# Kernel tuning notes

Hardware: AMD Instinct MI355X
Metric: run time of the kernel (lower is better)

The kernel has to match this reference:

```python
import jax, jax.numpy as jnp
import numpy as np

B, TX, TZ, DX, DZ, DATT, DMID, H, DOUT = 8, 1024, 1024, 1024, 1024, 64, 64, 16, 1024


def setup_inputs() -> dict:
    key = jax.random.key(0)
    ks = jax.random.split(key, 10)
    s = 0.02
    return {
        "x": jax.random.normal(ks[0], (B, TX, DX), jnp.float32),
        "z": jax.random.normal(ks[1], (B, TZ, DZ), jnp.float32),
        "Wq": jax.random.normal(ks[2], (H, DX, DATT), jnp.float32) * s,
        "bq": jax.random.normal(ks[3], (H, DATT), jnp.float32) * s,
        "Wk": jax.random.normal(ks[4], (H, DZ, DATT), jnp.float32) * s,
        "bk": jax.random.normal(ks[5], (H, DATT), jnp.float32) * s,
        "Wv": jax.random.normal(ks[6], (H, DZ, DMID), jnp.float32) * s,
        "bv": jax.random.normal(ks[7], (H, DMID), jnp.float32) * s,
        "Wp": jax.random.normal(ks[8], (H * DMID, DOUT), jnp.float32) * s,
        "bp": jax.random.normal(ks[9], (DOUT,), jnp.float32) * s,
        "mask": jnp.tril(jnp.ones((TX, TZ), dtype=bool)),  # causal
    }


def reference(x, z, Wq, bq, Wk, bk, Wv, bv, Wp, bp, mask):
    # Per-head projections (heads batched via stacked weights). bhxe = batch, head, x-pos, feat
    Q = jnp.einsum('bxd,hde->bhxe', x, Wq) + bq[None, :, None, :]
    K = jnp.einsum('bzd,hde->bhze', z, Wk) + bk[None, :, None, :]
    V = jnp.einsum('bzd,hde->bhze', z, Wv) + bv[None, :, None, :]
    # Scores, mask (set ~mask to -inf), then scale by 1/sqrt(Datt) (as original: mask before scale)
    S = jnp.einsum('bhxe,bhze->bhxz', Q, K)
    S = jnp.where(mask[None, None, :, :], S, -jnp.inf) * (1.0 / jnp.sqrt(jnp.asarray(DATT, S.dtype)))
    A = jax.nn.softmax(S, axis=-1)
    y = jnp.einsum('bhxz,bhze->bhxe', A, V)          # [B, H, Tx, Dmid]
    y_concat = y.transpose(0, 2, 1, 3).reshape(B, TX, H * DMID)  # concat heads
    return y_concat @ Wp + bp
```

## Files before the change

kernel.cpp:

```cpp
#include <hip/hip_runtime.h>
#include <stdint.h>


typedef float    f32x4  __attribute__((ext_vector_type(4)));
typedef __bf16   bf16x8 __attribute__((ext_vector_type(8)));
typedef unsigned short u16x4 __attribute__((ext_vector_type(4)));
typedef unsigned short u16x8 __attribute__((ext_vector_type(8)));

#define MASKNEG (-3.0e38f)
#define QSCALE_F (0.125f * 1.4426950408889634f)

__device__ __forceinline__ unsigned short f2bf(float f) {
  unsigned int u = __float_as_uint(f);
  u += 0x7fffu + ((u >> 16) & 1u);
  return (unsigned short)(u >> 16);
}

__device__ __forceinline__ void gload16(const void* g, void* s) {
  const __attribute__((address_space(1))) unsigned int* gp =
      (const __attribute__((address_space(1))) unsigned int*)(uintptr_t)g;
  __attribute__((address_space(3))) unsigned int* lp =
      (__attribute__((address_space(3))) unsigned int*)(unsigned int)(uintptr_t)s;
  __builtin_amdgcn_global_load_lds(gp, lp, 16, 0, 0);
}

__device__ __forceinline__ f32x4 mfma16(bf16x8 a, bf16x8 b, f32x4 c) {
  return __builtin_amdgcn_mfma_f32_16x16x32_bf16(a, b, c, 0, 0, 0);
}


__global__ __launch_bounds__(256) void k_cvt2(const float* __restrict__ x,
                                              const float* __restrict__ z,
                                              unsigned short* __restrict__ out) {
  int i = blockIdx.x * 256 + threadIdx.x;
  const int stride = gridDim.x * 256;
  for (; i < 2097152; i += stride) {
    const float* in = (i < 1048576) ? (x + (size_t)i * 8) : (z + (size_t)(i - 1048576) * 8);
    const f32x4* p = (const f32x4*)in;
    f32x4 a = p[0], b = p[1];
    u16x8 o;
    o[0] = f2bf(a[0]); o[1] = f2bf(a[1]); o[2] = f2bf(a[2]); o[3] = f2bf(a[3]);
    o[4] = f2bf(b[0]); o[5] = f2bf(b[1]); o[6] = f2bf(b[2]); o[7] = f2bf(b[3]);
    *(u16x8*)(out + (size_t)i * 8) = o;
  }
}

__global__ __launch_bounds__(256) void k_pack(const float* __restrict__ Wq,
                                              const float* __restrict__ Wk,
                                              const float* __restrict__ Wv,
                                              const float* __restrict__ Wp,
                                              unsigned short* __restrict__ Oq,
                                              unsigned short* __restrict__ Ok,
                                              unsigned short* __restrict__ Ov,
                                              unsigned short* __restrict__ Op) {
  __shared__ float tile[64][65];
  const int t = threadIdx.x;
  const int zid = blockIdx.z;
  if (zid < 3) {
    const float* W = zid == 0 ? Wq : (zid == 1 ? Wk : Wv);
    unsigned short* O = zid == 0 ? Oq : (zid == 1 ? Ok : Ov);
    const int h = blockIdx.x, d0 = blockIdx.y * 64;
    const int ee = t & 63, r0 = t >> 6;
#pragma unroll
    for (int dd = r0; dd < 64; dd += 4)
      tile[dd][ee] = W[(h * 1024 + d0 + dd) * 64 + ee];
    __syncthreads();
    const int d = t & 63, e0 = t >> 6;
#pragma unroll
    for (int e = e0; e < 64; e += 4)
      O[(h * 64 + e) * 1024 + d0 + d] = f2bf(tile[d][e]);
  } else {
    const int k0 = blockIdx.x * 64, n0 = blockIdx.y * 64;
    const int nn = t & 63, r0 = t >> 6;
#pragma unroll
    for (int kk = r0; kk < 64; kk += 4)
      tile[kk][nn] = Wp[(k0 + kk) * 1024 + n0 + nn];
    __syncthreads();
    const int kk = t & 63, e0 = t >> 6;
#pragma unroll
    for (int n2 = e0; n2 < 64; n2 += 4)
      Op[(n0 + n2) * 1024 + k0 + kk] = f2bf(tile[kk][n2]);
  }
}

__device__ __forceinline__ void gemm_body(const unsigned short* __restrict__ A,
                                          const unsigned short* __restrict__ Bt,
                                          const float* __restrict__ bias,
                                          void* __restrict__ outp,
                                          int mode, float oscale,
                                          int brow, int bcol,
                                          unsigned short* As, unsigned short* Bs) {
  const int tid = threadIdx.x;
  const int l = tid & 63, w = tid >> 6;
  const int lrow = l & 15, lk = l >> 4;
  const int wr = (w >> 1) * 128, wc = (w & 1) * 64;

  const int arow = tid >> 2;
  const int asrc = ((tid & 3) ^ ((arow >> 1) & 3)) * 8;
  const unsigned short* ag0 = A + (size_t)(brow + arow) * 1024 + asrc;
  const unsigned short* bg0 = Bt + (size_t)(bcol + arow) * 1024 + asrc;

  int aoff[8], boff[4];
#pragma unroll
  for (int m = 0; m < 8; m++) {
    int row = wr + m * 16 + lrow;
    aoff[m] = row * 64 + ((lk ^ ((row >> 1) & 3)) << 4);
  }
#pragma unroll
  for (int n = 0; n < 4; n++) {
    int col = wc + n * 16 + lrow;
    boff[n] = col * 64 + ((lk ^ ((col >> 1) & 3)) << 4);
  }

  f32x4 acc[8][4];
#pragma unroll
  for (int n = 0; n < 4; n++) {
    float bv = bias[bcol + wc + n * 16 + lrow];
#pragma unroll
    for (int m = 0; m < 8; m++) acc[m][n] = (f32x4){bv, bv, bv, bv};
  }

#define STAGE_G(kt, slot)                                                  \
  {                                                                        \
    char* asb = (char*)As + (slot) * 16384 + w * 1024;                     \
    char* bsb = (char*)Bs + (slot) * 8192 + w * 1024;                      \
    gload16(ag0 + (kt) * 32,          asb);                                \
    gload16(ag0 + (kt) * 32 + 65536,  asb + 4096);                         \
    gload16(ag0 + (kt) * 32 + 131072, asb + 8192);                         \
    gload16(ag0 + (kt) * 32 + 196608, asb + 12288);                        \
    gload16(bg0 + (kt) * 32,          bsb);                                \
    gload16(bg0 + (kt) * 32 + 65536,  bsb + 4096);                         \
  }

  STAGE_G(0, 0)
  STAGE_G(1, 1)
  asm volatile("s_waitcnt vmcnt(6)" ::: "memory");
  __builtin_amdgcn_s_barrier();
  __builtin_amdgcn_sched_barrier(0);

  int s0 = 0, s2 = 2;
#pragma unroll 1
  for (int kt = 0; kt < 32; kt++) {
    if (kt < 30) STAGE_G(kt + 2, s2)
    const char* ab = (const char*)As + s0 * 16384;
    const char* bb = (const char*)Bs + s0 * 8192;
    bf16x8 bfr[4];
#pragma unroll
    for (int n = 0; n < 4; n++) bfr[n] = *(const bf16x8*)(bb + boff[n]);
#pragma unroll
    for (int m = 0; m < 8; m++) {
      bf16x8 af = *(const bf16x8*)(ab + aoff[m]);
#pragma unroll
      for (int n = 0; n < 4; n++)
        acc[m][n] = mfma16(af, bfr[n], acc[m][n]);
    }
    if (kt < 31) {
      if (kt < 30) {
        asm volatile("s_waitcnt vmcnt(6)" ::: "memory");
      } else {
        asm volatile("s_waitcnt vmcnt(0)" ::: "memory");
      }
      __builtin_amdgcn_s_barrier();
      __builtin_amdgcn_sched_barrier(0);
    }
    s0 = (s0 == 2) ? 0 : s0 + 1;
    s2 = (s2 == 2) ? 0 : s2 + 1;
  }
#undef STAGE_G

  if (mode == 0) {
    unsigned short* C = (unsigned short*)outp;
#pragma unroll
    for (int m = 0; m < 8; m++) {
      int r = brow + wr + m * 16 + 4 * lk;
#pragma unroll
      for (int n = 0; n < 4; n++) {
        int c = bcol + wc + n * 16 + lrow;
        unsigned short* p = C + ((r >> 10) * 16 + (c >> 6)) * 65536 + (r & 1023) * 64 + (c & 63);
#pragma unroll
        for (int j = 0; j < 4; j++) p[j * 64] = f2bf(acc[m][n][j] * oscale);
      }
    }
  } else if (mode == 2) {
    unsigned short* C = (unsigned short*)outp;
#pragma unroll
    for (int m = 0; m < 8; m++) {
      int r = brow + wr + m * 16 + 4 * lk;
#pragma unroll
      for (int n = 0; n < 4; n++) {
        int c = bcol + wc + n * 16 + lrow;
        u16x4 o;
#pragma unroll
        for (int j = 0; j < 4; j++) o[j] = f2bf(acc[m][n][j]);
        *(u16x4*)(C + ((r >> 10) * 16 + (c >> 6)) * 65536 + (c & 63) * 1024 + (r & 1023)) = o;
      }
    }
  } else {
    float* C = (float*)outp;
#pragma unroll
    for (int m = 0; m < 8; m++) {
      int r = brow + wr + m * 16 + 4 * lk;
#pragma unroll
      for (int n = 0; n < 4; n++) {
        int c = bcol + wc + n * 16 + lrow;
#pragma unroll
        for (int j = 0; j < 4; j++) C[(r + j) * 1024 + c] = acc[m][n][j];
      }
    }
  }
}

__global__ __launch_bounds__(256, 2) void k_gemm_qkv(const unsigned short* __restrict__ Xb,
                                                     const unsigned short* __restrict__ Zb,
                                                     const unsigned short* __restrict__ Wqkv,
                                                     const float* __restrict__ bq,
                                                     const float* __restrict__ bk,
                                                     const float* __restrict__ bv,
                                                     unsigned short* __restrict__ Qp,
                                                     unsigned short* __restrict__ Kp,
                                                     unsigned short* __restrict__ Vtp) {
  __shared__ unsigned short As[24576];
  __shared__ unsigned short Bs[12288];
  const int brow = blockIdx.x * 256;
  const int cg = blockIdx.y;
  const int seg = cg >> 3;
  const int bcol = (cg & 7) * 128;
  const unsigned short* A = (seg == 0) ? Xb : Zb;
  const unsigned short* Bt = Wqkv + (size_t)seg * 1048576;
  const float* bias = (seg == 0) ? bq : (seg == 1 ? bk : bv);
  void* outp = (seg == 0) ? (void*)Qp : (seg == 1 ? (void*)Kp : (void*)Vtp);
  const int mode = (seg == 2) ? 2 : 0;
  const float oscale = (seg == 0) ? QSCALE_F : 1.0f;
  gemm_body(A, Bt, bias, outp, mode, oscale, brow, bcol, As, Bs);
}

__global__ __launch_bounds__(256, 2) void k_gemm(const unsigned short* __restrict__ A,
                                                 const unsigned short* __restrict__ Bt,
                                                 const float* __restrict__ bias,
                                                 void* __restrict__ outp,
                                                 int mode, float oscale) {
  __shared__ unsigned short As[24576];
  __shared__ unsigned short Bs[12288];
  gemm_body(A, Bt, bias, outp, mode, oscale, blockIdx.x * 256, blockIdx.y * 128, As, Bs);
}

__global__ __launch_bounds__(256) void k_attn(const unsigned short* __restrict__ Qh,
                                              const unsigned short* __restrict__ Kh,
                                              const unsigned short* __restrict__ Vth,
                                              unsigned short* __restrict__ Y) {
  __shared__ unsigned short Ks[8192];
  __shared__ unsigned short Vs[8192];
  __shared__ unsigned short Ps[8192];

  const int tid = threadIdx.x, l = tid & 63, w = tid >> 6;
  const int lrow = l & 15, lk = l >> 4;
  const int bh = blockIdx.y;
  const int pp = blockIdx.x;

  const unsigned short* Qb = Qh + bh * 65536;
  const unsigned short* Kb = Kh + bh * 65536;
  const unsigned short* Vb = Vth + bh * 65536;

  bf16x8 ones;
#pragma unroll
  for (int j = 0; j < 8; j++) ones[j] = (__bf16)1.0f;

  const int srow = tid >> 3;
  const int swz = ((tid & 7) ^ (srow & 7)) * 8;
  const unsigned short* kg0 = Kb + srow * 64 + swz;
  const unsigned short* kg1 = Kb + (srow + 32) * 64 + swz;
  const unsigned short* vg0 = Vb + srow * 1024 + swz;
  const unsigned short* vg1 = Vb + (srow + 32) * 1024 + swz;
  char* pw = (char*)Ps + w * 4096;

  const int b = bh >> 4, h = bh & 15;

#pragma unroll 1
  for (int half = 0; half < 2; half++) {
    const int qi = half == 0 ? (7 - pp) : pp;
    const int qw = qi * 128 + w * 32;
    const int qmax = qw + 31;

    bf16x8 qf[2][2];
#pragma unroll
    for (int qn = 0; qn < 2; qn++) {
      const unsigned short* qp = Qb + (qw + qn * 16 + lrow) * 64 + lk * 8;
      qf[qn][0] = *(const bf16x8*)qp;
      qf[qn][1] = *(const bf16x8*)(qp + 32);
    }

    f32x4 m[2], lsum[2], yacc[2][4];
#pragma unroll
    for (int qn = 0; qn < 2; qn++) {
      m[qn] = (f32x4){MASKNEG, MASKNEG, MASKNEG, MASKNEG};
      lsum[qn] = (f32x4){0.f, 0.f, 0.f, 0.f};
#pragma unroll
      for (int ef = 0; ef < 4; ef++) yacc[qn][ef] = (f32x4){0.f, 0.f, 0.f, 0.f};
    }

    const int nt = qi * 2 + 2;

    {
      char* ksb = (char*)Ks + w * 1024;
      char* vsb = (char*)Vs + w * 1024;
      gload16(kg0, ksb);
      gload16(kg1, ksb + 4096);
      gload16(vg0, vsb);
      gload16(vg1, vsb + 4096);
    }
    __syncthreads();

#pragma unroll 1
    for (int t = 0; t < nt; t++) {
      const int z0 = t * 64;
      const int cur = t & 1;
      if (t < nt - 1) {
        const int zn = (t + 1) * 64;
        char* ksb = (char*)Ks + (cur ^ 1) * 8192 + w * 1024;
        char* vsb = (char*)Vs + (cur ^ 1) * 8192 + w * 1024;
        gload16(kg0 + zn * 64, ksb);
        gload16(kg1 + zn * 64, ksb + 4096);
        gload16(vg0 + zn, vsb);
        gload16(vg1 + zn, vsb + 4096);
      }

      if (z0 <= qmax) {
        const char* kbase = (const char*)Ks + cur * 8192;
        const char* vbase = (const char*)Vs + cur * 8192;

        f32x4 s[2][4];
#pragma unroll
        for (int qn = 0; qn < 2; qn++)
#pragma unroll
          for (int zf = 0; zf < 4; zf++) s[qn][zf] = (f32x4){0.f, 0.f, 0.f, 0.f};
#pragma unroll
        for (int zf = 0; zf < 4; zf++) {
          int zr = zf * 16 + lrow;
#pragma unroll
          for (int kf = 0; kf < 2; kf++) {
            bf16x8 kfr = *(const bf16x8*)(kbase + zr * 128 + (((kf * 4 + lk) ^ (zr & 7)) << 4));
            s[0][zf] = mfma16(qf[0][kf], kfr, s[0][zf]);
            s[1][zf] = mfma16(qf[1][kf], kfr, s[1][zf]);
          }
        }

        if (z0 + 63 > qw) {
#pragma unroll
          for (int qn = 0; qn < 2; qn++) {
            int qbase = qw + qn * 16 + 4 * lk;
#pragma unroll
            for (int zf = 0; zf < 4; zf++) {
              int zg = z0 + zf * 16 + lrow;
#pragma unroll
              for (int j = 0; j < 4; j++)
                if (zg > qbase + j) s[qn][zf][j] = MASKNEG;
            }
          }
        }

#pragma unroll
        for (int qn = 0; qn < 2; qn++) {
#pragma unroll
          for (int j = 0; j < 4; j++) {
            float rm = fmaxf(fmaxf(s[qn][0][j], s[qn][1][j]), fmaxf(s[qn][2][j], s[qn][3][j]));
            rm = fmaxf(rm, __shfl_xor(rm, 1));
            rm = fmaxf(rm, __shfl_xor(rm, 2));
            rm = fmaxf(rm, __shfl_xor(rm, 4));
            rm = fmaxf(rm, __shfl_xor(rm, 8));
            float mn = fmaxf(m[qn][j], rm);
            float a = __builtin_amdgcn_exp2f(m[qn][j] - mn);
            m[qn][j] = mn;
            lsum[qn][j] *= a;
#pragma unroll
            for (int ef = 0; ef < 4; ef++) yacc[qn][ef][j] *= a;
#pragma unroll
            for (int zf = 0; zf < 4; zf++)
              s[qn][zf][j] = __builtin_amdgcn_exp2f(s[qn][zf][j] - mn);
          }

#pragma unroll
          for (int zf = 0; zf < 4; zf++) {
            int zc = zf * 16 + lrow;
            int zp = zc >> 3;
#pragma unroll
            for (int j = 0; j < 4; j++) {
              int q = 4 * lk + j;
              *(unsigned short*)(pw + (qn * 16 + q) * 128 + ((zp ^ (q & 7)) << 4) + (zc & 7) * 2)
                  = f2bf(s[qn][zf][j]);
            }
          }
        }

        asm volatile("s_waitcnt lgkmcnt(0)" ::: "memory");
        __builtin_amdgcn_sched_barrier(0);

        bf16x8 pf[2][2];
#pragma unroll
        for (int qn = 0; qn < 2; qn++)
#pragma unroll
          for (int kf = 0; kf < 2; kf++)
            pf[qn][kf] = *(const bf16x8*)(pw + (qn * 16 + lrow) * 128 + (((kf * 4 + lk) ^ (lrow & 7)) << 4));

#pragma unroll
        for (int qn = 0; qn < 2; qn++)
#pragma unroll
          for (int kf = 0; kf < 2; kf++)
            lsum[qn] = mfma16(pf[qn][kf], ones, lsum[qn]);

#pragma unroll
        for (int ef = 0; ef < 4; ef++) {
          int er = ef * 16 + lrow;
#pragma unroll
          for (int kf = 0; kf < 2; kf++) {
            bf16x8 vf = *(const bf16x8*)(vbase + er * 128 + (((kf * 4 + lk) ^ (er & 7)) << 4));
            yacc[0][ef] = mfma16(pf[0][kf], vf, yacc[0][ef]);
            yacc[1][ef] = mfma16(pf[1][kf], vf, yacc[1][ef]);
          }
        }
      }

      __syncthreads();
    }

#pragma unroll
    for (int qn = 0; qn < 2; qn++) {
      f32x4 rinv;
#pragma unroll
      for (int j = 0; j < 4; j++) rinv[j] = 1.0f / lsum[qn][j];
#pragma unroll
      for (int ef = 0; ef < 4; ef++) {
        int col = h * 64 + ef * 16 + lrow;
#pragma unroll
        for (int j = 0; j < 4; j++) {
          int x = qw + qn * 16 + lk * 4 + j;
          Y[(b * 1024 + x) * 1024 + col] = f2bf(yacc[qn][ef][j] * rinv[j]);
        }
      }
    }
  }
}

extern "C" void kernel_launch(void* const* d_in, const int* in_sizes, int n_in,
                              void* d_out, int out_size, void* d_ws, size_t ws_size,
                              hipStream_t stream) {
  const float* x  = (const float*)d_in[0];
  const float* z  = (const float*)d_in[1];
  const float* Wq = (const float*)d_in[2];
  const float* bq = (const float*)d_in[3];
  const float* Wk = (const float*)d_in[4];
  const float* bk = (const float*)d_in[5];
  const float* Wv = (const float*)d_in[6];
  const float* bv = (const float*)d_in[7];
  const float* Wp = (const float*)d_in[8];
  const float* bp = (const float*)d_in[9];
  (void)in_sizes; (void)n_in; (void)out_size; (void)ws_size;

  char* ws = (char*)d_ws;
  unsigned short* Xb  = (unsigned short*)(ws + 0);
  unsigned short* Zb  = (unsigned short*)(ws + 16777216);
  unsigned short* Wqt = (unsigned short*)(ws + 33554432);
  unsigned short* Wkt = (unsigned short*)(ws + 35651584);
  unsigned short* Wvt = (unsigned short*)(ws + 37748736);
  unsigned short* Wpt = (unsigned short*)(ws + 39845888);
  unsigned short* Qp  = (unsigned short*)(ws + 41943040);
  unsigned short* Kp  = (unsigned short*)(ws + 58720256);
  unsigned short* Vtp = (unsigned short*)(ws + 75497472);

  k_cvt2<<<dim3(2048), dim3(256), 0, stream>>>(x, z, Xb);
  k_pack<<<dim3(16, 16, 4), dim3(256), 0, stream>>>(Wq, Wk, Wv, Wp, Wqt, Wkt, Wvt, Wpt);

  k_gemm_qkv<<<dim3(32, 24), dim3(256), 0, stream>>>(Xb, Zb, Wqt, bq, bk, bv, Qp, Kp, Vtp);

  k_attn<<<dim3(4, 128), dim3(256), 0, stream>>>(Qp, Kp, Vtp, Xb );

  k_gemm<<<dim3(32, 8), dim3(256), 0, stream>>>(Xb, Wpt, bp, d_out, 3, 1.0f);
}
```

Before: 169.4 us.

## Widen attention KV tile to 128 and add lazy softmax rescaling

The attention kernel now processes 128 keys per tile instead of 64. This halves the number of tile iterations and block-wide barriers, and K/V shared buffers and swizzles are doubled to match. The online softmax now skips the max-update and rescale of the accumulators unless some row's max grows by more than 8 (in log2 units), which removes exp and multiply work on most tiles. Launch bounds request 2 blocks per SM. Costs are higher register and LDS pressure, plus a larger causal-masking waste on diagonal tiles.

After: 157.8 us. 6.8% less time.

```diff
diff --git a/kernel.cpp b/kernel.cpp
--- a/kernel.cpp
+++ b/kernel.cpp
@@ -244,12 +244,12 @@
   gemm_body(A, Bt, bias, outp, mode, oscale, blockIdx.x * 256, blockIdx.y * 128, As, Bs);
 }
 
-__global__ __launch_bounds__(256) void k_attn(const unsigned short* __restrict__ Qh,
-                                              const unsigned short* __restrict__ Kh,
-                                              const unsigned short* __restrict__ Vth,
-                                              unsigned short* __restrict__ Y) {
-  __shared__ unsigned short Ks[8192];
-  __shared__ unsigned short Vs[8192];
+__global__ __launch_bounds__(256, 2) void k_attn(const unsigned short* __restrict__ Qh,
+                                                 const unsigned short* __restrict__ Kh,
+                                                 const unsigned short* __restrict__ Vth,
+                                                 unsigned short* __restrict__ Y) {
+  __shared__ unsigned short Ks[16384];
+  __shared__ unsigned short Vs[16384];
   __shared__ unsigned short Ps[8192];
 
   const int tid = threadIdx.x, l = tid & 63, w = tid >> 6;
@@ -265,19 +265,27 @@
 #pragma unroll
   for (int j = 0; j < 8; j++) ones[j] = (__bf16)1.0f;
 
-  const int srow = tid >> 3;
-  const int swz = ((tid & 7) ^ (srow & 7)) * 8;
-  const unsigned short* kg0 = Kb + srow * 64 + swz;
-  const unsigned short* kg1 = Kb + (srow + 32) * 64 + swz;
-  const unsigned short* vg0 = Vb + srow * 1024 + swz;
-  const unsigned short* vg1 = Vb + (srow + 32) * 1024 + swz;
+  const int krl = l >> 3;
+  const int kgp = l & 7;
+  const unsigned short* kgsrc = Kb + (w * 32 + krl) * 64 + ((kgp ^ krl) * 8);
+  const int vrl = l >> 4;
+  const int vgp = l & 15;
+  const int vr0 = w * 16 + 0 * 4 + vrl;
+  const int vr1 = w * 16 + 1 * 4 + vrl;
+  const int vr2 = w * 16 + 2 * 4 + vrl;
+  const int vr3 = w * 16 + 3 * 4 + vrl;
+  const int voff0 = vr0 * 1024 + ((vgp ^ (vr0 & 15)) * 8);
+  const int voff1 = vr1 * 1024 + ((vgp ^ (vr1 & 15)) * 8);
+  const int voff2 = vr2 * 1024 + ((vgp ^ (vr2 & 15)) * 8);
+  const int voff3 = vr3 * 1024 + ((vgp ^ (vr3 & 15)) * 8);
+
   char* pw = (char*)Ps + w * 4096;
 
   const int b = bh >> 4, h = bh & 15;
 
 #pragma unroll 1
-  for (int half = 0; half < 2; half++) {
-    const int qi = half == 0 ? (7 - pp) : pp;
+  for (int hp = 0; hp < 2; hp++) {
+    const int qi = hp == 0 ? (7 - pp) : pp;
     const int qw = qi * 128 + w * 32;
     const int qmax = qw + 31;
 
@@ -298,43 +306,52 @@
       for (int ef = 0; ef < 4; ef++) yacc[qn][ef] = (f32x4){0.f, 0.f, 0.f, 0.f};
     }
 
-    const int nt = qi * 2 + 2;
+    const int nt = qi + 1;
 
     {
-      char* ksb = (char*)Ks + w * 1024;
-      char* vsb = (char*)Vs + w * 1024;
-      gload16(kg0, ksb);
-      gload16(kg1, ksb + 4096);
-      gload16(vg0, vsb);
-      gload16(vg1, vsb + 4096);
+      char* kb = (char*)Ks + w * 4096;
+      char* vb2 = (char*)Vs + w * 4096;
+      gload16(kgsrc + 0,    kb);
+      gload16(kgsrc + 512,  kb + 1024);
+      gload16(kgsrc + 1024, kb + 2048);
+      gload16(kgsrc + 1536, kb + 3072);
+      gload16(Vb + voff0, vb2);
+      gload16(Vb + voff1, vb2 + 1024);
+      gload16(Vb + voff2, vb2 + 2048);
+      gload16(Vb + voff3, vb2 + 3072);
     }
     __syncthreads();
 
 #pragma unroll 1
     for (int t = 0; t < nt; t++) {
-      const int z0 = t * 64;
+      const int z0 = t * 128;
       const int cur = t & 1;
       if (t < nt - 1) {
-        const int zn = (t + 1) * 64;
-        char* ksb = (char*)Ks + (cur ^ 1) * 8192 + w * 1024;
-        char* vsb = (char*)Vs + (cur ^ 1) * 8192 + w * 1024;
-        gload16(kg0 + zn * 64, ksb);
-        gload16(kg1 + zn * 64, ksb + 4096);
-        gload16(vg0 + zn, vsb);
-        gload16(vg1 + zn, vsb + 4096);
+        const int zn = (t + 1) * 128;
+        char* kb = (char*)Ks + (cur ^ 1) * 16384 + w * 4096;
+        char* vb2 = (char*)Vs + (cur ^ 1) * 16384 + w * 4096;
+        const unsigned short* kgt = kgsrc + zn * 64;
+        gload16(kgt + 0,    kb);
+        gload16(kgt + 512,  kb + 1024);
+        gload16(kgt + 1024, kb + 2048);
+        gload16(kgt + 1536, kb + 3072);
+        gload16(Vb + voff0 + zn, vb2);
+        gload16(Vb + voff1 + zn, vb2 + 1024);
+        gload16(Vb + voff2 + zn, vb2 + 2048);
+        gload16(Vb + voff3 + zn, vb2 + 3072);
       }
 
       if (z0 <= qmax) {
-        const char* kbase = (const char*)Ks + cur * 8192;
-        const char* vbase = (const char*)Vs + cur * 8192;
-
-        f32x4 s[2][4];
+        const char* kbase = (const char*)Ks + cur * 16384;
+        const char* vbase = (const char*)Vs + cur * 16384;
+
+        f32x4 s[2][8];
 #pragma unroll
         for (int qn = 0; qn < 2; qn++)
 #pragma unroll
-          for (int zf = 0; zf < 4; zf++) s[qn][zf] = (f32x4){0.f, 0.f, 0.f, 0.f};
-#pragma unroll
-        for (int zf = 0; zf < 4; zf++) {
+          for (int zf = 0; zf < 8; zf++) s[qn][zf] = (f32x4){0.f, 0.f, 0.f, 0.f};
+#pragma unroll
+        for (int zf = 0; zf < 8; zf++) {
           int zr = zf * 16 + lrow;
 #pragma unroll
           for (int kf = 0; kf < 2; kf++) {
@@ -344,12 +361,12 @@
           }
         }
 
-        if (z0 + 63 > qw) {
+        if (z0 + 127 > qw) {
 #pragma unroll
           for (int qn = 0; qn < 2; qn++) {
             int qbase = qw + qn * 16 + 4 * lk;
 #pragma unroll
-            for (int zf = 0; zf < 4; zf++) {
+            for (int zf = 0; zf < 8; zf++) {
               int zg = z0 + zf * 16 + lrow;
 #pragma unroll
               for (int j = 0; j < 4; j++)
@@ -360,61 +377,86 @@
 
 #pragma unroll
         for (int qn = 0; qn < 2; qn++) {
+          f32x4 rm4 = s[qn][0];
+#pragma unroll
+          for (int zf = 1; zf < 8; zf++)
+#pragma unroll
+            for (int j = 0; j < 4; j++) rm4[j] = fmaxf(rm4[j], s[qn][zf][j]);
 #pragma unroll
           for (int j = 0; j < 4; j++) {
-            float rm = fmaxf(fmaxf(s[qn][0][j], s[qn][1][j]), fmaxf(s[qn][2][j], s[qn][3][j]));
-            rm = fmaxf(rm, __shfl_xor(rm, 1));
-            rm = fmaxf(rm, __shfl_xor(rm, 2));
-            rm = fmaxf(rm, __shfl_xor(rm, 4));
-            rm = fmaxf(rm, __shfl_xor(rm, 8));
-            float mn = fmaxf(m[qn][j], rm);
-            float a = __builtin_amdgcn_exp2f(m[qn][j] - mn);
-            m[qn][j] = mn;
-            lsum[qn][j] *= a;
-#pragma unroll
-            for (int ef = 0; ef < 4; ef++) yacc[qn][ef][j] *= a;
-#pragma unroll
-            for (int zf = 0; zf < 4; zf++)
-              s[qn][zf][j] = __builtin_amdgcn_exp2f(s[qn][zf][j] - mn);
+            float r = rm4[j];
+            r = fmaxf(r, __shfl_xor(r, 1));
+            r = fmaxf(r, __shfl_xor(r, 2));
+            r = fmaxf(r, __shfl_xor(r, 4));
+            r = fmaxf(r, __shfl_xor(r, 8));
+            rm4[j] = r;
           }
-
-#pragma unroll
-          for (int zf = 0; zf < 4; zf++) {
-            int zc = zf * 16 + lrow;
-            int zp = zc >> 3;
+          int trig = (rm4[0] > m[qn][0] + 8.f) | (rm4[1] > m[qn][1] + 8.f) |
+                     (rm4[2] > m[qn][2] + 8.f) | (rm4[3] > m[qn][3] + 8.f);
+          if (__any(trig)) {
 #pragma unroll
             for (int j = 0; j < 4; j++) {
-              int q = 4 * lk + j;
-              *(unsigned short*)(pw + (qn * 16 + q) * 128 + ((zp ^ (q & 7)) << 4) + (zc & 7) * 2)
-                  = f2bf(s[qn][zf][j]);
+              float mn = fmaxf(m[qn][j], rm4[j]);
+              float a = __builtin_amdgcn_exp2f(m[qn][j] - mn);
+              m[qn][j] = mn;
+              lsum[qn][j] *= a;
+#pragma unroll
+              for (int ef = 0; ef < 4; ef++) yacc[qn][ef][j] *= a;
             }
           }
+#pragma unroll
+          for (int zf = 0; zf < 8; zf++)
+#pragma unroll
+            for (int j = 0; j < 4; j++)
+              s[qn][zf][j] = __builtin_amdgcn_exp2f(s[qn][zf][j] - m[qn][j]);
         }
 
-        asm volatile("s_waitcnt lgkmcnt(0)" ::: "memory");
-        __builtin_amdgcn_sched_barrier(0);
-
-        bf16x8 pf[2][2];
-#pragma unroll
-        for (int qn = 0; qn < 2; qn++)
-#pragma unroll
-          for (int kf = 0; kf < 2; kf++)
-            pf[qn][kf] = *(const bf16x8*)(pw + (qn * 16 + lrow) * 128 + (((kf * 4 + lk) ^ (lrow & 7)) << 4));
-
-#pragma unroll
-        for (int qn = 0; qn < 2; qn++)
-#pragma unroll
-          for (int kf = 0; kf < 2; kf++)
-            lsum[qn] = mfma16(pf[qn][kf], ones, lsum[qn]);
-
-#pragma unroll
-        for (int ef = 0; ef < 4; ef++) {
-          int er = ef * 16 + lrow;
-#pragma unroll
-          for (int kf = 0; kf < 2; kf++) {
-            bf16x8 vf = *(const bf16x8*)(vbase + er * 128 + (((kf * 4 + lk) ^ (er & 7)) << 4));
-            yacc[0][ef] = mfma16(pf[0][kf], vf, yacc[0][ef]);
-            yacc[1][ef] = mfma16(pf[1][kf], vf, yacc[1][ef]);
+#pragma unroll
+        for (int hf = 0; hf < 2; hf++) {
+          if (z0 + hf * 64 <= qmax) {
+#pragma unroll
+            for (int qn = 0; qn < 2; qn++) {
+#pragma unroll
+              for (int zf2 = 0; zf2 < 4; zf2++) {
+                int zfg = hf * 4 + zf2;
+                int zc = zf2 * 16 + lrow;
+                int zp = zc >> 3;
+#pragma unroll
+                for (int j = 0; j < 4; j++) {
+                  int q = 4 * lk + j;
+                  *(unsigned short*)(pw + (qn * 16 + q) * 128 + ((zp ^ (q & 7)) << 4) + (zc & 7) * 2)
+                      = f2bf(s[qn][zfg][j]);
+                }
+              }
+            }
+
+            asm volatile("s_waitcnt lgkmcnt(0)" ::: "memory");
+            __builtin_amdgcn_sched_barrier(0);
+
+            bf16x8 pf[2][2];
+#pragma unroll
+            for (int qn = 0; qn < 2; qn++)
+#pragma unroll
+              for (int kf = 0; kf < 2; kf++)
+                pf[qn][kf] = *(const bf16x8*)(pw + (qn * 16 + lrow) * 128 + (((kf * 4 + lk) ^ (lrow & 7)) << 4));
+
+#pragma unroll
+            for (int qn = 0; qn < 2; qn++)
+#pragma unroll
+              for (int kf = 0; kf < 2; kf++)
+                lsum[qn] = mfma16(pf[qn][kf], ones, lsum[qn]);
+
+#pragma unroll
+            for (int ef = 0; ef < 4; ef++) {
+              int er = ef * 16 + lrow;
+#pragma unroll
+              for (int kf = 0; kf < 2; kf++) {
+                int g = hf * 8 + kf * 4 + lk;
+                bf16x8 vf = *(const bf16x8*)(vbase + er * 256 + ((g ^ (er & 15)) << 4));
+                yacc[0][ef] = mfma16(pf[0][kf], vf, yacc[0][ef]);
+                yacc[1][ef] = mfma16(pf[1][kf], vf, yacc[1][ef]);
+              }
+            }
           }
         }
       }
```
